# Performance work log

Measured on AMD Instinct MI355X. Metric: run time of the kernel, lower is better.

Reference implementation:

```python
import jax, jax.numpy as jnp
import numpy as np

EPS = 1e-5

def layer_norm(x, g, b):
    mu = jnp.mean(x, axis=-1, keepdims=True)
    var = jnp.var(x, axis=-1, keepdims=True)
    return (x - mu) * jax.lax.rsqrt(var + EPS) * g + b

def rel_shift(x):
    # x: [N, H, T1, T2] with T2 = 2*T1 - 1 -> [N, H, T1, T1]
    N, H, T1, T2 = x.shape
    zp = jnp.zeros((N, H, T1, 1), dtype=x.dtype)
    xp = jnp.concatenate([zp, x], axis=-1).reshape(N, H, T2 + 1, T1)
    x = xp[:, :, 1:, :].reshape(N, H, T1, T2)
    return x[:, :, :, : T2 // 2 + 1]

def setup_inputs() -> dict:
    B, T, D, Hh = 8, 1024, 512, 8
    dk = D // Hh
    P = 2 * T - 1
    key = jax.random.key(0)
    ks = jax.random.split(key, 12)
    s = 0.02
    return {
        "q": jax.random.normal(ks[0], (B, T, D), jnp.float32),
        "k": jax.random.normal(ks[1], (B, T, D), jnp.float32),
        "v": jax.random.normal(ks[2], (B, T, D), jnp.float32),
        "pos_emb": jax.random.normal(ks[3], (1, P, D), jnp.float32),
        "mask": jnp.ones((B, T, T), jnp.int32),
        "ln_q_g": jnp.ones((D,), jnp.float32), "ln_q_b": jnp.zeros((D,), jnp.float32),
        "ln_k_g": jnp.ones((D,), jnp.float32), "ln_k_b": jnp.zeros((D,), jnp.float32),
        "ln_v_g": jnp.ones((D,), jnp.float32), "ln_v_b": jnp.zeros((D,), jnp.float32),
        "w_q": jax.random.normal(ks[4], (D, D), jnp.float32) * s,   # [out, in]
        "w_k": jax.random.normal(ks[5], (D, D), jnp.float32) * s,
        "w_v": jax.random.normal(ks[6], (D, D), jnp.float32) * s,
        "w_pos": jax.random.normal(ks[7], (D, D), jnp.float32) * s,
        "w_fc": jax.random.normal(ks[8], (D, D), jnp.float32) * s,
        "pos_bias_u": jax.random.normal(ks[9], (Hh, dk), jnp.float32) * s,
        "pos_bias_v": jax.random.normal(ks[10], (Hh, dk), jnp.float32) * s,
    }

def reference(q, k, v, pos_emb, mask, ln_q_g, ln_q_b, ln_k_g, ln_k_b, ln_v_g, ln_v_b,
              w_q, w_k, w_v, w_pos, w_fc, pos_bias_u, pos_bias_v):
    B, T, D = q.shape
    H, dk = pos_bias_u.shape
    scale = 1.0 / np.sqrt(dk).astype(np.float32)
    residual = q
    qn = layer_norm(q, ln_q_g, ln_q_b)
    kn = layer_norm(k, ln_k_g, ln_k_b)
    vn = layer_norm(v, ln_v_g, ln_v_b)
    # projections (torch Linear: x @ W^T), reshape to [B, H, T, dk]
    qh = (qn @ w_q.T).reshape(B, T, H, dk)                      # [B, T, H, dk]
    kh = (kn @ w_k.T).reshape(B, T, H, dk).transpose(0, 2, 1, 3)  # [B, H, T, dk]
    vh = (vn @ w_v.T).reshape(B, T, H, dk).transpose(0, 2, 1, 3)
    p = (pos_emb @ w_pos.T).reshape(pos_emb.shape[0], -1, H, dk).transpose(0, 2, 1, 3)  # [1, H, P, dk]
    q_u = (qh + pos_bias_u).transpose(0, 2, 1, 3)  # [B, H, T, dk]
    q_v = (qh + pos_bias_v).transpose(0, 2, 1, 3)
    matrix_ac = jnp.einsum('bhqd,bhkd->bhqk', q_u, kh)          # [B, H, T, T]
    matrix_bd = jnp.einsum('bhqd,nhpd->bhqp', q_v, p)           # [B, H, T, 2T-1]
    matrix_bd = rel_shift(matrix_bd)                             # [B, H, T, T]
    scores = (matrix_ac + matrix_bd) * scale
    m = (mask[:, None, :, :] == 0)                               # [B, 1, T, T]
    scores = jnp.where(m, -jnp.inf, scores)
    attn = jax.nn.softmax(scores, axis=-1)
    attn = jnp.where(m, 0.0, attn)
    out = jnp.einsum('bhqk,bhkd->bhqd', attn, vh)                # [B, H, T, dk]
    out = out.transpose(0, 2, 1, 3).reshape(B, T, H * dk)
    out = out @ w_fc.T + residual
    return out, attn
```

## Files before the change

kernel.cpp:

```cpp
#include <hip/hip_runtime.h>

constexpr int cT  = 1024;
constexpr int cD  = 512;
constexpr int cDK = 64;
constexpr int cP  = 2047;
constexpr int PBS = 1040;

typedef __attribute__((ext_vector_type(8))) short short8;
typedef __attribute__((ext_vector_type(4))) float floatx4;

#define MFMA16(a,b,c) __builtin_amdgcn_mfma_f32_16x16x32_bf16((a),(b),(c),0,0,0)
#define SWZ(i,j) ((j) ^ ((((i) >> 2) & 3) << 3))

__device__ __forceinline__ unsigned short f2bf(float f){
  union { float f; unsigned int u; } x; x.f = f;
  unsigned int r = x.u + 0x7fffu + ((x.u >> 16) & 1u);
  return (unsigned short)(r >> 16);
}
__device__ __forceinline__ float bf2f(unsigned short h){
  union { unsigned int u; float f; } x; x.u = ((unsigned int)h) << 16;
  return x.f;
}
__device__ __forceinline__ short8 ld8(const unsigned short* p){
  return *(const short8*)p;
}

struct LN3 { const float* x[3]; const float* g[3]; const float* b[3]; unsigned short* y[3]; };
__global__ void __launch_bounds__(256) ln3_kernel(LN3 a)
{
  __shared__ float red[8];
  const int z = blockIdx.y, r = blockIdx.x;
  const float* x = a.x[z]; const float* g = a.g[z]; const float* b = a.b[z];
  unsigned short* y = a.y[z];
  const float2 v = ((const float2*)(x + (size_t)r * cD))[threadIdx.x];
  float s = v.x + v.y, sq = v.x * v.x + v.y * v.y;
  #pragma unroll
  for (int o = 32; o; o >>= 1){ s += __shfl_xor(s, o); sq += __shfl_xor(sq, o); }
  const int w = threadIdx.x >> 6;
  if ((threadIdx.x & 63) == 0){ red[w * 2] = s; red[w * 2 + 1] = sq; }
  __syncthreads();
  s  = red[0] + red[2] + red[4] + red[6];
  sq = red[1] + red[3] + red[5] + red[7];
  const float mu  = s * (1.0f / cD);
  const float var = sq * (1.0f / cD) - mu * mu;
  const float rs  = rsqrtf(var + 1e-5f);
  const int c = threadIdx.x * 2;
  const unsigned int o0 = f2bf((v.x - mu) * rs * g[c]     + b[c]);
  const unsigned int o1 = f2bf((v.y - mu) * rs * g[c + 1] + b[c + 1]);
  ((unsigned int*)(y + (size_t)r * cD))[threadIdx.x] = o0 | (o1 << 16);
}

struct Ptr5 { const float* p[5]; };
__global__ void __launch_bounds__(256) cast5_kernel(Ptr5 s, unsigned short* __restrict__ d){
  const int idx = blockIdx.x * 256 + threadIdx.x;
  const int seg = idx >> 18, off = idx & 262143;
  d[idx] = f2bf(s.p[seg][off]);
}
__global__ void __launch_bounds__(256) cast1_kernel(const float* __restrict__ s,
    unsigned short* __restrict__ d, int n){
  const int idx = blockIdx.x * 256 + threadIdx.x;
  if (idx < n) d[idx] = f2bf(s[idx]);
}

__global__ void __launch_bounds__(256) maskbits_kernel(
    const int* __restrict__ mask, unsigned int* __restrict__ bm)
{
  const int row = blockIdx.x * 4 + (threadIdx.x >> 6);
  const int lane = threadIdx.x & 63;
  #pragma unroll
  for (int ii = 0; ii < 16; ii++){
    const int m = mask[(size_t)row * cT + ii * 64 + lane];
    const unsigned long long bal = __ballot(m != 0);
    if (lane == 0)       bm[row * 32 + ii * 2]     = (unsigned int)bal;
    else if (lane == 32) bm[row * 32 + ii * 2 + 1] = (unsigned int)(bal >> 32);
  }
}

__global__ void __launch_bounds__(256) gemm512_kernel(
    const unsigned short* __restrict__ A0, const unsigned short* __restrict__ W0,
    int M, int mode, float scaleA, unsigned short* __restrict__ outb,
    float* __restrict__ outf, const float* __restrict__ residual)
{
  const int z = blockIdx.z;
  const unsigned short* A = A0 + (size_t)z * 4194304;
  const unsigned short* W = W0 + (size_t)z * 262144;
  unsigned short* outz = outb ? outb + (size_t)z * 4194304 : outb;
  const float sA = (z == 0) ? scaleA : 1.0f;
  const int n0 = blockIdx.x * 128, m0 = blockIdx.y * 128;
  const int wave = threadIdx.x >> 6, lane = threadIdx.x & 63;
  const int wr = wave >> 1, wc = wave & 1;
  const int l15 = lane & 15, lq = lane >> 4;
  const int mb = m0 + wr * 64, nb = n0 + wc * 64;
  floatx4 acc[4][4];
  #pragma unroll
  for (int i = 0; i < 4; i++)
    #pragma unroll
    for (int j = 0; j < 4; j++) acc[i][j] = (floatx4){0.f, 0.f, 0.f, 0.f};
  for (int k0 = 0; k0 < 512; k0 += 32){
    short8 af[4], bf[4];
    #pragma unroll
    for (int i = 0; i < 4; i++){
      int row = mb + i * 16 + l15; if (row >= M) row = M - 1;
      af[i] = ld8(A + (size_t)row * 512 + k0 + lq * 8);
      const int col = nb + i * 16 + l15;
      bf[i] = ld8(W + (size_t)col * 512 + k0 + lq * 8);
    }
    #pragma unroll
    for (int i = 0; i < 4; i++)
      #pragma unroll
      for (int j = 0; j < 4; j++)
        acc[i][j] = MFMA16(af[i], bf[j], acc[i][j]);
  }
  #pragma unroll
  for (int i = 0; i < 4; i++){
    #pragma unroll
    for (int j = 0; j < 4; j++){
      #pragma unroll
      for (int r = 0; r < 4; r++){
        const int row = mb + i * 16 + lq * 4 + r;
        const int col = nb + j * 16 + l15;
        if (row >= M) continue;
        const float val = acc[i][j][r] * sA;
        if (mode == 0){
          const int bb = row >> 10, t = row & 1023, h = col >> 6, d = col & 63;
          outz[(((size_t)(bb * 8 + h) * 1024 + t) << 6) + d] = f2bf(val);
        } else if (mode == 1){
          const int h = col >> 6, d = col & 63;
          outz[(((size_t)h * 2047 + row) << 6) + d] = f2bf(val);
        } else {
          const size_t idx = (size_t)row * 512 + col;
          outf[idx] = val + residual[idx];
        }
      }
    }
  }
}

__global__ void __launch_bounds__(256) transpose_v_kernel(
    const unsigned short* __restrict__ vh, unsigned short* __restrict__ vt)
{
  __shared__ unsigned short tile[64][65];
  const int bh = blockIdx.x, t0 = blockIdx.y * 64;
  const unsigned short* src = vh + ((size_t)bh * cT + t0) * cDK;
  #pragma unroll
  for (int i = 0; i < 16; i++){
    const int idx = threadIdx.x + i * 256;
    tile[idx >> 6][idx & 63] = src[idx];
  }
  __syncthreads();
  unsigned short* dst = vt + (size_t)bh * cDK * cT + t0;
  #pragma unroll
  for (int i = 0; i < 16; i++){
    const int idx = threadIdx.x + i * 256;
    const int d = idx >> 6, t = idx & 63;
    dst[(size_t)d * cT + t] = tile[t][d];
  }
}

__global__ void __launch_bounds__(256) dot_bias_kernel(
    const unsigned short* __restrict__ X, const float* __restrict__ bias,
    float* __restrict__ out, int rows, int hdiv, float scale)
{
  const int row = blockIdx.x * 4 + (threadIdx.x >> 6);
  const int lane = threadIdx.x & 63;
  if (row >= rows) return;
  const int h = (row / hdiv) & 7;
  float s = bf2f(X[(size_t)row * 64 + lane]) * bias[h * 64 + lane];
  #pragma unroll
  for (int o = 32; o; o >>= 1) s += __shfl_xor(s, o);
  if (lane == 0) out[row] = s * scale;
}

__global__ void __launch_bounds__(512, 4) attn_kernel(
    const unsigned short* __restrict__ qh, const unsigned short* __restrict__ kh,
    const unsigned short* __restrict__ vt, const unsigned short* __restrict__ pproj,
    const float* __restrict__ ubias, const float* __restrict__ vbias,
    const unsigned int* __restrict__ bm, float* __restrict__ attn_out,
    unsigned short* __restrict__ out_h)
{
  __shared__ float sc[16 * cT];
  unsigned short* pbuf = (unsigned short*)sc;
  const int bh = blockIdx.x, b = bh >> 3, h = bh & 7;
  const int q0 = blockIdx.y * 16;
  const int wave = threadIdx.x >> 6, lane = threadIdx.x & 63;
  const int l15 = lane & 15, lq = lane >> 4;
  const unsigned short* Q  = qh + (size_t)bh * cT * cDK;
  const unsigned short* Kp = kh + (size_t)bh * cT * cDK;
  const unsigned short* Pt = pproj + (size_t)h * cP * cDK;

  const short8 qf0 = ld8(Q + (size_t)(q0 + l15) * cDK + lq * 8);
  const short8 qf1 = ld8(Q + (size_t)(q0 + l15) * cDK + 32 + lq * 8);

  for (int jt = wave; jt < 64; jt += 8){
    const short8 kf0 = ld8(Kp + (size_t)(jt * 16 + l15) * cDK + lq * 8);
    const short8 kf1 = ld8(Kp + (size_t)(jt * 16 + l15) * cDK + 32 + lq * 8);
    floatx4 acc = (floatx4){0.f, 0.f, 0.f, 0.f};
    acc = MFMA16(qf0, kf0, acc);
    acc = MFMA16(qf1, kf1, acc);
    const int jb = jt * 16 + l15;
    #pragma unroll
    for (int r = 0; r < 4; r++){
      const int i = lq * 4 + r;
      sc[i * cT + (jb ^ (lq << 3))] = acc[r];
    }
  }
  __syncthreads();

  const int w0 = (cT - 1) - q0 - 15;
  for (int ct = wave; ct < 65; ct += 8){
    const int c = ct * 16 + l15;
    int prow = w0 + c; if (prow > cP - 1) prow = cP - 1;
    const short8 pf0 = ld8(Pt + (size_t)prow * cDK + lq * 8);
    const short8 pf1 = ld8(Pt + (size_t)prow * cDK + 32 + lq * 8);
    floatx4 acc = (floatx4){0.f, 0.f, 0.f, 0.f};
    acc = MFMA16(qf0, pf0, acc);
    acc = MFMA16(qf1, pf1, acc);
    #pragma unroll
    for (int r = 0; r < 4; r++){
      const int i = lq * 4 + r;
      const int j = c - 15 + i;
      if (j >= 0 && j < cT) sc[i * cT + SWZ(i, j)] += acc[r];
    }
  }
  __syncthreads();

  const float* ub = ubias + (size_t)bh * cT;
  const float* vb = vbias + (size_t)h * cP;
  for (int p = 0; p < 2; p++){
    const int i = p * 8 + wave;
    const int qrow = q0 + i;
    const unsigned int* bmr = bm + ((size_t)b * cT + qrow) * 32;
    float vals[16];
    float mx = -INFINITY;
    #pragma unroll
    for (int ii = 0; ii < 16; ii++){
      const int j = lane + ii * 64;
      float s = sc[i * cT + SWZ(i, j)] + ub[j] + vb[j + (cT - 1) - qrow];
      const unsigned int mw = bmr[ii * 2 + (lane >> 5)];
      if (((mw >> (lane & 31)) & 1u) == 0u) s = -INFINITY;
      vals[ii] = s;
      mx = fmaxf(mx, s);
    }
    #pragma unroll
    for (int o = 32; o; o >>= 1) mx = fmaxf(mx, __shfl_xor(mx, o));
    float sum = 0.f;
    #pragma unroll
    for (int ii = 0; ii < 16; ii++){
      const float e = (vals[ii] == -INFINITY) ? 0.f : __expf(vals[ii] - mx);
      vals[ii] = e; sum += e;
    }
    #pragma unroll
    for (int o = 32; o; o >>= 1) sum += __shfl_xor(sum, o);
    const float ri = sum > 0.f ? 1.f / sum : 0.f;
    __syncthreads();
    float* arow = attn_out + ((size_t)bh * cT + qrow) * cT;
    #pragma unroll
    for (int ii = 0; ii < 16; ii++){
      const int j = lane + ii * 64;
      const float pr = vals[ii] * ri;
      __builtin_nontemporal_store(pr, arow + j);
      pbuf[i * PBS + j] = f2bf(pr);
    }
  }
  __syncthreads();

  const unsigned short* V = vt + (size_t)bh * cDK * cT;
  const int d0 = (wave & 3) * 16;
  const int kh2 = wave >> 2;
  floatx4 acc = (floatx4){0.f, 0.f, 0.f, 0.f};
  for (int ks = 0; ks < 16; ks++){
    const int j0 = (kh2 * 16 + ks) * 32;
    const short8 vf = ld8(V + (size_t)(d0 + l15) * cT + j0 + lq * 8);
    const short8 af = ld8(pbuf + l15 * PBS + j0 + lq * 8);
    acc = MFMA16(af, vf, acc);
  }
  float* red4 = sc + 10240;
  if (kh2 == 1) *(floatx4*)(red4 + ((wave & 3) * 256 + lane * 4)) = acc;
  __syncthreads();
  if (kh2 == 0){
    acc += *(const floatx4*)(red4 + ((wave & 3) * 256 + lane * 4));
    #pragma unroll
    for (int r = 0; r < 4; r++){
      const int i = lq * 4 + r;
      out_h[((size_t)b * cT + q0 + i) * cD + h * cDK + d0 + l15] = f2bf(acc[r]);
    }
  }
}

extern "C" void kernel_launch(void* const* d_in, const int* in_sizes, int n_in,
                              void* d_out, int out_size, void* d_ws, size_t ws_size,
                              hipStream_t stream)
{
  const float* q    = (const float*)d_in[0];
  const float* k    = (const float*)d_in[1];
  const float* v    = (const float*)d_in[2];
  const float* pe   = (const float*)d_in[3];
  const int*   mask = (const int*)d_in[4];
  const float* lnqg = (const float*)d_in[5];
  const float* lnqb = (const float*)d_in[6];
  const float* lnkg = (const float*)d_in[7];
  const float* lnkb = (const float*)d_in[8];
  const float* lnvg = (const float*)d_in[9];
  const float* lnvb = (const float*)d_in[10];
  const float* wq   = (const float*)d_in[11];
  const float* wk   = (const float*)d_in[12];
  const float* wv   = (const float*)d_in[13];
  const float* wpos = (const float*)d_in[14];
  const float* wfc  = (const float*)d_in[15];
  const float* pbu  = (const float*)d_in[16];
  const float* pbv  = (const float*)d_in[17];

  float* out_f  = (float*)d_out;
  float* attn_f = out_f + (size_t)8 * 1024 * 512;

  unsigned char* scr = (unsigned char*)attn_f;
  size_t soff = 0;
  auto salloc = [&](size_t bytes){ void* p = scr + soff; soff += (bytes + 255) & ~(size_t)255; return p; };
  unsigned short* qn   = (unsigned short*)salloc((size_t)8192 * 512 * 2);
  unsigned short* kn   = (unsigned short*)salloc((size_t)8192 * 512 * 2);
  unsigned short* vn   = (unsigned short*)salloc((size_t)8192 * 512 * 2);
  unsigned short* pe_b = (unsigned short*)salloc((size_t)2047 * 512 * 2);
  (void)kn; (void)vn;

  unsigned char* ws = (unsigned char*)d_ws;
  size_t off = 0;
  auto alloc = [&](size_t bytes){ void* p = ws + off; off += (bytes + 255) & ~(size_t)255; return p; };
  unsigned short* w5_b = (unsigned short*)alloc(5 * 512 * 512 * 2);
  unsigned short* qhb  = (unsigned short*)alloc((size_t)8192 * 512 * 2);
  unsigned short* khb  = (unsigned short*)alloc((size_t)8192 * 512 * 2);
  unsigned short* vhb  = (unsigned short*)alloc((size_t)8192 * 512 * 2);
  unsigned short* vtb  = (unsigned short*)alloc((size_t)8192 * 512 * 2);
  unsigned short* ppb  = (unsigned short*)alloc((size_t)8 * 2047 * 64 * 2);
  float*          ub   = (float*)alloc((size_t)8 * 8 * 1024 * 4);
  float*          vbias= (float*)alloc((size_t)8 * 2047 * 4);
  unsigned short* ohb  = (unsigned short*)alloc((size_t)8192 * 512 * 2);
  unsigned int*   bmask= (unsigned int*)alloc((size_t)8192 * 32 * 4);
  (void)ws_size; (void)n_in; (void)in_sizes; (void)out_size;

  Ptr5 c5; c5.p[0] = wq; c5.p[1] = wk; c5.p[2] = wv; c5.p[3] = wpos; c5.p[4] = wfc;
  cast5_kernel<<<5120, 256, 0, stream>>>(c5, w5_b);
  cast1_kernel<<<4094, 256, 0, stream>>>(pe, pe_b, 2047 * 512);
  maskbits_kernel<<<2048, 256, 0, stream>>>(mask, bmask);

  LN3 l3;
  l3.x[0] = q; l3.x[1] = k; l3.x[2] = v;
  l3.g[0] = lnqg; l3.g[1] = lnkg; l3.g[2] = lnvg;
  l3.b[0] = lnqb; l3.b[1] = lnkb; l3.b[2] = lnvb;
  l3.y[0] = qn; l3.y[1] = kn; l3.y[2] = vn;
  ln3_kernel<<<dim3(8192, 3), 256, 0, stream>>>(l3);

  gemm512_kernel<<<dim3(4, 64, 3), 256, 0, stream>>>(qn, w5_b, 8192, 0, 0.125f,
                                                     qhb, nullptr, nullptr);
  gemm512_kernel<<<dim3(4, 16, 1), 256, 0, stream>>>(pe_b, w5_b + 3 * 262144, 2047, 1, 1.0f,
                                                     ppb, nullptr, nullptr);

  transpose_v_kernel<<<dim3(64, 16), 256, 0, stream>>>(vhb, vtb);

  dot_bias_kernel<<<16384, 256, 0, stream>>>(khb, pbu, ub, 65536, 1024, 0.125f);
  dot_bias_kernel<<<4094, 256, 0, stream>>>(ppb, pbv, vbias, 16376, 2047, 0.125f);

  attn_kernel<<<dim3(64, 64), 512, 0, stream>>>(qhb, khb, vtb, ppb, ub, vbias,
                                                bmask, attn_f, ohb);

  gemm512_kernel<<<dim3(4, 64, 1), 256, 0, stream>>>(ohb, w5_b + 4 * 262144, 8192, 2, 1.0f,
                                                     nullptr, out_f, q);
}
```

Before: 719.4 us.

## Restructure softmax to contiguous per-lane columns with vectorized stores and fused biases

Moves the u/v bias addition into the QK score write, changes the LDS swizzle so each lane can read 16 contiguous score columns, and has each wave handle two rows with lane-contiguous chunks. The attention output is written as 128-bit nontemporal stores, bf16 probabilities are packed into 128-bit LDS writes, and __syncthreads is replaced by a raw waitcnt+barrier. The aim is fewer scattered global stores and mask loads and cheaper barriers, at the cost of more registers (32 live values per lane) and a more complex swizzle.

```diff
diff --git a/kernel.cpp b/kernel.cpp
--- a/kernel.cpp
+++ b/kernel.cpp
@@ -8,9 +8,14 @@
 
 typedef __attribute__((ext_vector_type(8))) short short8;
 typedef __attribute__((ext_vector_type(4))) float floatx4;
+typedef __attribute__((ext_vector_type(4))) unsigned int uintx4;
 
 #define MFMA16(a,b,c) __builtin_amdgcn_mfma_f32_16x16x32_bf16((a),(b),(c),0,0,0)
-#define SWZ(i,j) ((j) ^ ((((i) >> 2) & 3) << 3))
+#define PHYS(i,j) (((j) ^ ((j) >> 4)) ^ ((((i) >> 2) & 3) << 3))
+
+__device__ __forceinline__ void bar_lds(){
+  asm volatile("s_waitcnt lgkmcnt(0)\n\ts_barrier" ::: "memory");
+}
 
 __device__ __forceinline__ unsigned short f2bf(float f){
   union { float f; unsigned int u; } x; x.f = f;
@@ -187,6 +192,8 @@
   const unsigned short* Q  = qh + (size_t)bh * cT * cDK;
   const unsigned short* Kp = kh + (size_t)bh * cT * cDK;
   const unsigned short* Pt = pproj + (size_t)h * cP * cDK;
+  const float* ub = ubias + (size_t)bh * cT;
+  const float* vb = vbias + (size_t)h * cP;
 
   const short8 qf0 = ld8(Q + (size_t)(q0 + l15) * cDK + lq * 8);
   const short8 qf1 = ld8(Q + (size_t)(q0 + l15) * cDK + 32 + lq * 8);
@@ -198,13 +205,14 @@
     acc = MFMA16(qf0, kf0, acc);
     acc = MFMA16(qf1, kf1, acc);
     const int jb = jt * 16 + l15;
+    const float ubv = ub[jb];
     #pragma unroll
     for (int r = 0; r < 4; r++){
       const int i = lq * 4 + r;
-      sc[i * cT + (jb ^ (lq << 3))] = acc[r];
-    }
-  }
-  __syncthreads();
+      sc[i * cT + PHYS(i, jb)] = acc[r] + ubv + vb[jb + (cT - 1) - (q0 + i)];
+    }
+  }
+  bar_lds();
 
   const int w0 = (cT - 1) - q0 - 15;
   for (int ct = wave; ct < 65; ct += 8){
@@ -219,26 +227,26 @@
     for (int r = 0; r < 4; r++){
       const int i = lq * 4 + r;
       const int j = c - 15 + i;
-      if (j >= 0 && j < cT) sc[i * cT + SWZ(i, j)] += acc[r];
-    }
-  }
-  __syncthreads();
-
-  const float* ub = ubias + (size_t)bh * cT;
-  const float* vb = vbias + (size_t)h * cP;
-  for (int p = 0; p < 2; p++){
-    const int i = p * 8 + wave;
+      if (j >= 0 && j < cT) sc[i * cT + PHYS(i, j)] += acc[r];
+    }
+  }
+  bar_lds();
+
+  const int jb = lane * 16;
+  float vals[2][16];
+  float rcp[2];
+  #pragma unroll
+  for (int rr = 0; rr < 2; rr++){
+    const int i = wave * 2 + rr;
     const int qrow = q0 + i;
-    const unsigned int* bmr = bm + ((size_t)b * cT + qrow) * 32;
-    float vals[16];
+    const unsigned int mw = bm[((size_t)b * cT + qrow) * 32 + (lane >> 1)];
+    const int msh = (lane & 1) * 16;
     float mx = -INFINITY;
     #pragma unroll
     for (int ii = 0; ii < 16; ii++){
-      const int j = lane + ii * 64;
-      float s = sc[i * cT + SWZ(i, j)] + ub[j] + vb[j + (cT - 1) - qrow];
-      const unsigned int mw = bmr[ii * 2 + (lane >> 5)];
-      if (((mw >> (lane & 31)) & 1u) == 0u) s = -INFINITY;
-      vals[ii] = s;
+      float s = sc[i * cT + PHYS(i, jb + ii)];
+      if (((mw >> (msh + ii)) & 1u) == 0u) s = -INFINITY;
+      vals[rr][ii] = s;
       mx = fmaxf(mx, s);
     }
     #pragma unroll
@@ -246,23 +254,40 @@
     float sum = 0.f;
     #pragma unroll
     for (int ii = 0; ii < 16; ii++){
-      const float e = (vals[ii] == -INFINITY) ? 0.f : __expf(vals[ii] - mx);
-      vals[ii] = e; sum += e;
+      const float e = (vals[rr][ii] == -INFINITY) ? 0.f : __expf(vals[rr][ii] - mx);
+      vals[rr][ii] = e; sum += e;
     }
     #pragma unroll
     for (int o = 32; o; o >>= 1) sum += __shfl_xor(sum, o);
-    const float ri = sum > 0.f ? 1.f / sum : 0.f;
-    __syncthreads();
-    float* arow = attn_out + ((size_t)bh * cT + qrow) * cT;
-    #pragma unroll
-    for (int ii = 0; ii < 16; ii++){
-      const int j = lane + ii * 64;
-      const float pr = vals[ii] * ri;
-      __builtin_nontemporal_store(pr, arow + j);
-      pbuf[i * PBS + j] = f2bf(pr);
-    }
-  }
-  __syncthreads();
+    rcp[rr] = sum > 0.f ? 1.f / sum : 0.f;
+  }
+  bar_lds();
+  #pragma unroll
+  for (int rr = 0; rr < 2; rr++){
+    const int i = wave * 2 + rr;
+    const int qrow = q0 + i;
+    #pragma unroll
+    for (int ii = 0; ii < 16; ii++) vals[rr][ii] *= rcp[rr];
+    uintx4 w0v, w1v;
+    #pragma unroll
+    for (int t = 0; t < 4; t++)
+      w0v[t] = (unsigned int)f2bf(vals[rr][2 * t]) |
+               ((unsigned int)f2bf(vals[rr][2 * t + 1]) << 16);
+    #pragma unroll
+    for (int t = 0; t < 4; t++)
+      w1v[t] = (unsigned int)f2bf(vals[rr][8 + 2 * t]) |
+               ((unsigned int)f2bf(vals[rr][8 + 2 * t + 1]) << 16);
+    uintx4* pw = (uintx4*)(pbuf + (size_t)i * PBS + jb);
+    pw[0] = w0v; pw[1] = w1v;
+    float* arow = attn_out + ((size_t)bh * cT + qrow) * cT + jb;
+    #pragma unroll
+    for (int t = 0; t < 4; t++){
+      floatx4 pv = (floatx4){ vals[rr][4 * t], vals[rr][4 * t + 1],
+                              vals[rr][4 * t + 2], vals[rr][4 * t + 3] };
+      __builtin_nontemporal_store(pv, (floatx4*)arow + t);
+    }
+  }
+  bar_lds();
 
   const unsigned short* V = vt + (size_t)bh * cDK * cT;
   const int d0 = (wave & 3) * 16;
@@ -276,7 +301,7 @@
   }
   float* red4 = sc + 10240;
   if (kh2 == 1) *(floatx4*)(red4 + ((wave & 3) * 256 + lane * 4)) = acc;
-  __syncthreads();
+  bar_lds();
   if (kh2 == 0){
     acc += *(const floatx4*)(red4 + ((wave & 3) * 256 + lane * 4));
     #pragma unroll
```

Measured after the change: 903.5 us. +25.6%, slower.
